# Kernel tuning notes

Measured on AMD Instinct MI355X. Metric: run time of the kernel, lower is better.

Reference implementation:

```python
import jax, jax.numpy as jnp
import numpy as np

# Concrete MACE layer instantiation: hidden irreps = F x (0e + 1o)
N, E, F, R, S, H = 20000, 320000, 64, 8, 10, 64
P = 5                      # CG tensor-product paths for (0e+1o) x (0e+1o)
AVG_NEIGH = 16.0
INV_SQRT3 = 1.0 / np.sqrt(3.0).astype(np.float32)
INV_SQRT2 = 1.0 / np.sqrt(2.0).astype(np.float32)


def setup_inputs() -> dict:
    key = jax.random.key(0)
    ks = jax.random.split(key, 24)
    rn = lambda k, shp, sc=1.0: jax.random.normal(k, shp, dtype=jnp.float32) * sc
    y = jax.random.normal(ks[2], (E, 3), dtype=jnp.float32)
    Y1 = y / jnp.linalg.norm(y, axis=-1, keepdims=True)  # unit spherical harmonics l=1
    return dict(
        s=rn(ks[0], (N, F)),                 # scalar node feats (0e)
        v=rn(ks[1], (N, F, 3)),              # vector node feats (1o)
        Y1=Y1,
        edge_feats=rn(ks[3], (E, R)),        # radial basis
        node_specie=jax.random.randint(ks[4], (N,), 0, S),
        senders=jax.random.randint(ks[5], (E,), 0, N),
        receivers=jax.random.randint(ks[6], (E,), 0, N),
        W_lin_s=rn(ks[7], (F, F), F ** -0.5),
        W_lin_v=rn(ks[8], (F, F), F ** -0.5),
        W_sc_s=rn(ks[9], (S, F, F), F ** -0.5),   # species-dependent skip
        W_sc_v=rn(ks[10], (S, F, F), F ** -0.5),
        W_rad1=rn(ks[11], (R, H), R ** -0.5),     # radial MLP
        W_rad2=rn(ks[12], (H, P * F), H ** -0.5),
        W_int_s=rn(ks[13], (F, F), F ** -0.5),    # post-aggregation linear
        W_int_v=rn(ks[14], (F, F), F ** -0.5),
        w_prod_s=rn(ks[15], (S, 5, F)),           # product-basis species weights (0e out)
        w_prod_v=rn(ks[16], (S, 4, F)),           # product-basis species weights (1o out)
        W_prod_s=rn(ks[17], (F, F), F ** -0.5),
        W_prod_v=rn(ks[18], (F, F), F ** -0.5),
        W_read=rn(ks[19], (F, 1), F ** -0.5),     # linear readout to 0e
    )


def reference(s, v, Y1, edge_feats, node_specie, senders, receivers,
              W_lin_s, W_lin_v, W_sc_s, W_sc_v, W_rad1, W_rad2,
              W_int_s, W_int_v, w_prod_s, w_prod_v, W_prod_s, W_prod_v, W_read):
    n = s.shape[0]
    # --- interaction block: linear up ---
    s1 = s @ W_lin_s                              # [N,F]
    v1 = jnp.einsum('nfc,fg->ngc', v, W_lin_v)    # [N,F,3]
    # species-dependent residual skip connection
    sc_s = jnp.einsum('nf,nfg->ng', s, W_sc_s[node_specie])
    sc_v = jnp.einsum('nfc,nfg->ngc', v, W_sc_v[node_specie])
    # radial MLP -> per-edge, per-path, per-channel tensor-product weights
    h = jax.nn.silu(edge_feats @ W_rad1)
    tw = (h @ W_rad2).reshape(-1, P, F)           # [E,P,F]
    # gather sender features onto edges
    ss = s1[senders]                              # [E,F]
    vs = v1[senders]                              # [E,F,3]
    # CG tensor product with edge spherical harmonics (Y0 == const)
    dot = jnp.einsum('efc,ec->ef', vs, Y1)        # 1o x 1o -> 0e
    crs = jnp.cross(vs, Y1[:, None, :])           # 1o x 1o -> 1o
    m_s = tw[:, 0] * ss + tw[:, 1] * dot * INV_SQRT3                     # [E,F]
    m_v = (tw[:, 2, :, None] * ss[..., None] * Y1[:, None, :]            # 0e x 1o -> 1o
           + tw[:, 3, :, None] * vs                                      # 1o x 0e -> 1o
           + tw[:, 4, :, None] * crs * INV_SQRT2)                        # [E,F,3]
    # scatter-sum over edges to receiver nodes
    A_s = jax.ops.segment_sum(m_s, receivers, num_segments=n)
    A_v = jax.ops.segment_sum(m_v, receivers, num_segments=n)
    # linear to interaction irreps + neighbor normalization (epsilon is None)
    inv = 1.0 / jnp.sqrt(jnp.asarray(AVG_NEIGH, s.dtype))
    A_s = (A_s @ W_int_s) * inv
    A_v = jnp.einsum('nfc,fg->ngc', A_v, W_int_v) * inv
    # --- equivariant product basis (symmetric contraction, correlation=3) ---
    ws = w_prod_s[node_specie]                    # [N,5,F]
    wv = w_prod_v[node_specie]                    # [N,4,F]
    d = jnp.sum(A_v * A_v, axis=-1)               # v.v invariant [N,F]
    B_s = (ws[:, 0] * A_s + ws[:, 1] * A_s * A_s + ws[:, 2] * d
           + ws[:, 3] * A_s ** 3 + ws[:, 4] * A_s * d)
    B_v = (wv[:, 0] + wv[:, 1] * A_s + wv[:, 2] * A_s * A_s + wv[:, 3] * d)[..., None] * A_v
    s_out = B_s @ W_prod_s + sc_s
    v_out = jnp.einsum('nfc,fg->ngc', B_v, W_prod_v) + sc_v
    # --- linear readout (not last layer): invariant per-node output ---
    node_outputs = s_out @ W_read                 # [N,1]
    return node_outputs, s_out, v_out
```

## Files before the change

### kernel.cpp

```cpp
#include <hip/hip_runtime.h>

#define NNODES 20000
#define NEDGES 320000
#define NTILES 1260

typedef __attribute__((ext_vector_type(8))) short short8;
typedef __attribute__((ext_vector_type(4))) float float4v;
typedef _Float16 half2v __attribute__((ext_vector_type(2)));

#define CW2   0
#define CWls  2560
#define CWlv  3072
#define CWis  3584
#define CWiv  4096
#define CWps  4608
#define CWpv  5120
#define CWss  5632
#define CWsv  10752
#define NCHUNK_TOT 15872

__device__ __forceinline__ float bitsf(unsigned u){ union{unsigned u; float f;} x; x.u=u; return x.f; }
__device__ __forceinline__ float b2f(unsigned short u){ return bitsf(((unsigned)u)<<16); }
__device__ __forceinline__ unsigned short f2b(float f){
    union{float f; unsigned u;} x; x.f=f;
    unsigned r = x.u + 0x7fffu + ((x.u>>16)&1u);
    return (unsigned short)(r>>16);
}
__device__ __forceinline__ short8 pack8(const float* f){
    short8 r;
    #pragma unroll
    for (int j=0;j<8;++j) r[j] = (short)f2b(f[j]);
    return r;
}

__constant__ float kINV_SQRT3 = 0.5773502691896258f;
__constant__ float kINV_SQRT2 = 0.7071067811865476f;
__constant__ float kINV_AVG   = 0.25f;

__global__ __launch_bounds__(256) void kprep(
    const int* __restrict__ specie,
    const float* __restrict__ Wr2,
    const float* __restrict__ Wls, const float* __restrict__ Wlv,
    const float* __restrict__ Wis, const float* __restrict__ Wiv,
    const float* __restrict__ Wps, const float* __restrict__ Wpv,
    const float* __restrict__ Wss, const float* __restrict__ Wsv,
    unsigned short* __restrict__ P,
    int* __restrict__ perm, int* __restrict__ tspec)
{
    const int tid = threadIdx.x;
    if (blockIdx.x == 0){
        __shared__ int cnt[10], base[10], ntl[10], cur[10];
        if (tid < 10) cnt[tid] = 0;
        __syncthreads();
        for (int n = tid; n < NNODES; n += 256) atomicAdd(&cnt[specie[n]], 1);
        __syncthreads();
        if (tid == 0){
            int b = 0;
            for (int sp = 0; sp < 10; ++sp){
                base[sp] = b; cur[sp] = b;
                ntl[sp] = (cnt[sp] + 15) >> 4;
                b += ntl[sp] << 4;
            }
        }
        __syncthreads();
        for (int i = tid; i < NTILES*16; i += 256) perm[i] = -1;
        for (int t = tid; t < NTILES; t += 256){
            int sp = 0;
            #pragma unroll
            for (int k = 0; k < 10; ++k)
                if (t >= (base[k] >> 4) && t < (base[k] >> 4) + ntl[k]) sp = k;
            tspec[t] = sp;
        }
        __syncthreads();
        for (int n = tid; n < NNODES; n += 256){
            int slot = atomicAdd(&cur[specie[n]], 1);
            perm[slot] = n;
        }
        return;
    }
    const int c = (blockIdx.x - 1)*256 + tid;
    if (c >= NCHUNK_TOT) return;
    unsigned short t[8];
    if (c < 2560){
        const int nt = c >> 7, ks = (c >> 6) & 1, ln = c & 63;
        const int col = nt*16 + (ln & 15);
        const int jb  = ks*32 + ((ln >> 4) & 3)*8;
        #pragma unroll
        for (int jj = 0; jj < 8; ++jj) t[jj] = f2b(Wr2[(jb+jj)*320 + col]);
    } else {
        int c2 = c - 2560;
        const float* src;
        if      (c2 <  512){ src = Wls; }
        else if (c2 < 1024){ src = Wlv; c2 -= 512; }
        else if (c2 < 1536){ src = Wis; c2 -= 1024; }
        else if (c2 < 2048){ src = Wiv; c2 -= 1536; }
        else if (c2 < 2560){ src = Wps; c2 -= 2048; }
        else if (c2 < 3072){ src = Wpv; c2 -= 2560; }
        else if (c2 < 8192){ src = Wss; c2 -= 3072; }
        else               { src = Wsv; c2 -= 8192; }
        const int grp = c2 >> 9, loc = c2 & 511;
        const int nt = loc >> 7, ks = (loc >> 6) & 1, ln = loc & 63;
        const int col  = nt*16 + (ln & 15);
        const int row0 = grp*64 + ks*32 + ((ln>>4)&3)*8;
        #pragma unroll
        for (int jj = 0; jj < 8; ++jj) t[jj] = f2b(src[(row0+jj)*64 + col]);
    }
    unsigned* d = (unsigned*)(P + (size_t)c*8);
    d[0] = (unsigned)t[0] | ((unsigned)t[1]<<16);
    d[1] = (unsigned)t[2] | ((unsigned)t[3]<<16);
    d[2] = (unsigned)t[4] | ((unsigned)t[5]<<16);
    d[3] = (unsigned)t[6] | ((unsigned)t[7]<<16);
}

__global__ __launch_bounds__(256) void knodeA2(
    const float* __restrict__ s, const float* __restrict__ v,
    const unsigned short* __restrict__ P,
    unsigned short* __restrict__ s1, unsigned short* __restrict__ v1,
    float4v* __restrict__ AhZ)
{
    float4v zz = {0.f,0.f,0.f,0.f};
    for (int i = blockIdx.x*256 + threadIdx.x; i < NNODES*32; i += 313*256) AhZ[i] = zz;

    const int w = threadIdx.x >> 6, lane = threadIdx.x & 63;
    const int t = blockIdx.x*4 + w;
    if (t >= 1250) return;
    const int mcol = lane & 15, quad = lane >> 4;
    const int node = t*16 + mcol;
    const short8* PB = (const short8*)P;

    short8 fS[2], fV[3][2];
    #pragma unroll
    for (int ks = 0; ks < 2; ++ks){
        const int k0 = ks*32 + quad*8;
        float ts[8];
        { float4v a = *(const float4v*)&s[node*64 + k0];
          float4v b = *(const float4v*)&s[node*64 + k0 + 4];
          #pragma unroll
          for (int j = 0; j < 4; ++j){ ts[j] = a[j]; ts[4+j] = b[j]; } }
        fS[ks] = pack8(ts);
        float tv[24];
        #pragma unroll
        for (int q = 0; q < 6; ++q){
            float4v x = *(const float4v*)&v[(node*64 + k0)*3 + q*4];
            #pragma unroll
            for (int j = 0; j < 4; ++j) tv[q*4+j] = x[j];
        }
        #pragma unroll
        for (int c = 0; c < 3; ++c){
            float tc[8];
            #pragma unroll
            for (int j = 0; j < 8; ++j) tc[j] = tv[j*3 + c];
            fV[c][ks] = pack8(tc);
        }
    }
    float4v z = {0.f,0.f,0.f,0.f};
    #pragma unroll
    for (int nt = 0; nt < 4; ++nt){
        float4v aS = __builtin_amdgcn_mfma_f32_16x16x32_bf16(fS[0], PB[CWls+(nt*2+0)*64+lane], z, 0,0,0);
        aS = __builtin_amdgcn_mfma_f32_16x16x32_bf16(fS[1], PB[CWls+(nt*2+1)*64+lane], aS, 0,0,0);
        float4v aV[3];
        #pragma unroll
        for (int c = 0; c < 3; ++c){
            aV[c] = __builtin_amdgcn_mfma_f32_16x16x32_bf16(fV[c][0], PB[CWlv+(nt*2+0)*64+lane], z, 0,0,0);
            aV[c] = __builtin_amdgcn_mfma_f32_16x16x32_bf16(fV[c][1], PB[CWlv+(nt*2+1)*64+lane], aV[c], 0,0,0);
        }
        const int g = nt*16 + mcol;
        #pragma unroll
        for (int r = 0; r < 4; ++r){
            const int nr = t*16 + quad*4 + r;
            s1[nr*64 + g] = f2b(aS[r]);
            #pragma unroll
            for (int c = 0; c < 3; ++c) v1[(nr*3+c)*64 + g] = f2b(aV[c][r]);
        }
    }
}

__global__ __launch_bounds__(256) void kedge2(
    const float* __restrict__ Y1, const float* __restrict__ ef,
    const int* __restrict__ senders, const int* __restrict__ receivers,
    const float* __restrict__ Wr1, const unsigned short* __restrict__ W2s,
    const unsigned short* __restrict__ s1, const unsigned short* __restrict__ v1,
    half2v* __restrict__ Ah)
{
    __shared__ unsigned short hlds[64*72];
    __shared__ unsigned short twlds[64*330];
    const int lane = threadIdx.x & 63;
    const int w    = threadIdx.x >> 6;
    const int ew   = blockIdx.x*64 + w*16;

    float ef0 = ef[ew*8 + lane];
    float ef1 = ef[ew*8 + 64 + lane];
    float w1r[8];
    #pragma unroll
    for (int r = 0; r < 8; ++r) w1r[r] = Wr1[r*64 + lane];
    float yreg  = (lane < 48) ? Y1[ew*3 + lane] : 0.f;
    int sndreg  = (lane < 16) ? senders[ew + lane]   : 0;
    int rcvreg  = (lane < 16) ? receivers[ew + lane] : 0;
    #pragma unroll
    for (int e16 = 0; e16 < 16; ++e16){
        float src = (e16 < 8) ? ef0 : ef1;
        float hj = 0.f;
        #pragma unroll
        for (int r = 0; r < 8; ++r) hj += __shfl(src, (e16&7)*8 + r) * w1r[r];
        hj = hj / (1.f + __expf(-hj));
        hlds[(w*16 + e16)*72 + lane] = f2b(hj);
    }
    __syncthreads();

    short8 a0 = *(const short8*)&hlds[(w*16 + (lane&15))*72 +      (lane>>4)*8];
    short8 a1 = *(const short8*)&hlds[(w*16 + (lane&15))*72 + 32 + (lane>>4)*8];
    float4v acc[20];
    #pragma unroll
    for (int nt = 0; nt < 20; ++nt){
        short8 b0 = *(const short8*)&W2s[((nt*2+0)*64 + lane)*8];
        short8 b1 = *(const short8*)&W2s[((nt*2+1)*64 + lane)*8];
        float4v z = {0.f, 0.f, 0.f, 0.f};
        acc[nt] = __builtin_amdgcn_mfma_f32_16x16x32_bf16(a0, b0, z, 0, 0, 0);
        acc[nt] = __builtin_amdgcn_mfma_f32_16x16x32_bf16(a1, b1, acc[nt], 0, 0, 0);
    }
    #pragma unroll
    for (int nt = 0; nt < 20; ++nt){
        const int col = nt*16 + (lane & 15);
        #pragma unroll
        for (int r = 0; r < 4; ++r){
            const int erow = w*16 + (lane>>4)*4 + r;
            twlds[erow*330 + col] = f2b(acc[nt][r]);
        }
    }

    for (int e16 = 0; e16 < 16; ++e16){
        const int erow = w*16 + e16;
        float tw0 = b2f(twlds[erow*330 +   0 + lane]);
        float tw1 = b2f(twlds[erow*330 +  64 + lane]);
        float tw2 = b2f(twlds[erow*330 + 128 + lane]);
        float tw3 = b2f(twlds[erow*330 + 192 + lane]);
        float tw4 = b2f(twlds[erow*330 + 256 + lane]);
        const int snd = __shfl(sndreg, e16);
        const int rcv = __shfl(rcvreg, e16);
        float y0 = __shfl(yreg, e16*3+0);
        float y1 = __shfl(yreg, e16*3+1);
        float y2 = __shfl(yreg, e16*3+2);
        float ss  = b2f(s1[snd*64 + lane]);
        float vs0 = b2f(v1[(snd*3+0)*64 + lane]);
        float vs1 = b2f(v1[(snd*3+1)*64 + lane]);
        float vs2 = b2f(v1[(snd*3+2)*64 + lane]);
        float dot = vs0*y0 + vs1*y1 + vs2*y2;
        float c0 = vs1*y2 - vs2*y1;
        float c1 = vs2*y0 - vs0*y2;
        float c2 = vs0*y1 - vs1*y0;
        float ms  = tw0*ss + tw1*dot*kINV_SQRT3;
        float t2s = tw2*ss, t4 = tw4*kINV_SQRT2;
        float mv0 = t2s*y0 + tw3*vs0 + t4*c0;
        float mv1 = t2s*y1 + tw3*vs1 + t4*c1;
        float mv2 = t2s*y2 + tw3*vs2 + t4*c2;
        half2v p01 = { (_Float16)ms,  (_Float16)mv0 };
        half2v p23 = { (_Float16)mv1, (_Float16)mv2 };
        __builtin_amdgcn_global_atomic_fadd_v2f16(&Ah[rcv*128 + lane],      p01);
        __builtin_amdgcn_global_atomic_fadd_v2f16(&Ah[rcv*128 + 64 + lane], p23);
    }
}

__global__ __launch_bounds__(256) void knodeC2(
    const float* __restrict__ s, const float* __restrict__ v,
    const half2v* __restrict__ Ah,
    const unsigned short* __restrict__ P,
    const int* __restrict__ perm, const int* __restrict__ tspec,
    const float* __restrict__ wps, const float* __restrict__ wpv,
    const float* __restrict__ Wread,
    float* __restrict__ out)
{
    __shared__ unsigned short Bt[4][4][16*72];
    const int w = threadIdx.x >> 6, lane = threadIdx.x & 63;
    const int t = blockIdx.x*4 + w;
    if (t >= NTILES) return;
    const int mcol = lane & 15, quad = lane >> 4;
    const int spec = tspec[t];
    const int nA   = perm[t*16 + mcol];
    const short8* PB = (const short8*)P;
    const int sb = CWss + spec*512, vb = CWsv + spec*512;

    short8 fAs[2], fAv[3][2], fS[2], fV[3][2];
    if (nA >= 0){
        #pragma unroll
        for (int ks = 0; ks < 2; ++ks){
            const int k0 = ks*32 + quad*8;
            half2v pa[8], pb[8];
            *(float4v*)&pa[0] = *(const float4v*)&Ah[nA*128 + k0];
            *(float4v*)&pa[4] = *(const float4v*)&Ah[nA*128 + k0 + 4];
            *(float4v*)&pb[0] = *(const float4v*)&Ah[nA*128 + 64 + k0];
            *(float4v*)&pb[4] = *(const float4v*)&Ah[nA*128 + 64 + k0 + 4];
            float as_[8], a0_[8], a1_[8], a2_[8];
            #pragma unroll
            for (int j = 0; j < 8; ++j){
                as_[j] = (float)pa[j].x; a0_[j] = (float)pa[j].y;
                a1_[j] = (float)pb[j].x; a2_[j] = (float)pb[j].y;
            }
            fAs[ks] = pack8(as_); fAv[0][ks] = pack8(a0_);
            fAv[1][ks] = pack8(a1_); fAv[2][ks] = pack8(a2_);
            float ts[8];
            { float4v a = *(const float4v*)&s[nA*64 + k0];
              float4v b = *(const float4v*)&s[nA*64 + k0 + 4];
              #pragma unroll
              for (int j = 0; j < 4; ++j){ ts[j] = a[j]; ts[4+j] = b[j]; } }
            fS[ks] = pack8(ts);
            float tv[24];
            #pragma unroll
            for (int q = 0; q < 6; ++q){
                float4v x = *(const float4v*)&v[(nA*64 + k0)*3 + q*4];
                #pragma unroll
                for (int j = 0; j < 4; ++j) tv[q*4+j] = x[j];
            }
            #pragma unroll
            for (int c = 0; c < 3; ++c){
                float tc[8];
                #pragma unroll
                for (int j = 0; j < 8; ++j) tc[j] = tv[j*3 + c];
                fV[c][ks] = pack8(tc);
            }
        }
    } else {
        short8 z8 = {};
        #pragma unroll
        for (int ks = 0; ks < 2; ++ks){
            fAs[ks] = z8; fS[ks] = z8;
            #pragma unroll
            for (int c = 0; c < 3; ++c){ fAv[c][ks] = z8; fV[c][ks] = z8; }
        }
    }

    float4v z = {0.f,0.f,0.f,0.f};
    float4v scS[4], scV[3][4];
    #pragma unroll
    for (int nt = 0; nt < 4; ++nt){
        float4v Ais = __builtin_amdgcn_mfma_f32_16x16x32_bf16(fAs[0], PB[CWis+(nt*2+0)*64+lane], z, 0,0,0);
        Ais = __builtin_amdgcn_mfma_f32_16x16x32_bf16(fAs[1], PB[CWis+(nt*2+1)*64+lane], Ais, 0,0,0);
        float4v Aiv[3];
        #pragma unroll
        for (int c = 0; c < 3; ++c){
            Aiv[c] = __builtin_amdgcn_mfma_f32_16x16x32_bf16(fAv[c][0], PB[CWiv+(nt*2+0)*64+lane], z, 0,0,0);
            Aiv[c] = __builtin_amdgcn_mfma_f32_16x16x32_bf16(fAv[c][1], PB[CWiv+(nt*2+1)*64+lane], Aiv[c], 0,0,0);
        }
        scS[nt] = __builtin_amdgcn_mfma_f32_16x16x32_bf16(fS[0], PB[sb+(nt*2+0)*64+lane], z, 0,0,0);
        scS[nt] = __builtin_amdgcn_mfma_f32_16x16x32_bf16(fS[1], PB[sb+(nt*2+1)*64+lane], scS[nt], 0,0,0);
        #pragma unroll
        for (int c = 0; c < 3; ++c){
            scV[c][nt] = __builtin_amdgcn_mfma_f32_16x16x32_bf16(fV[c][0], PB[vb+(nt*2+0)*64+lane], z, 0,0,0);
            scV[c][nt] = __builtin_amdgcn_mfma_f32_16x16x32_bf16(fV[c][1], PB[vb+(nt*2+1)*64+lane], scV[c][nt], 0,0,0);
        }
        const int g = nt*16 + mcol;
        float w0 = wps[spec*320 +   0 + g], w1 = wps[spec*320 +  64 + g];
        float w2 = wps[spec*320 + 128 + g], w3 = wps[spec*320 + 192 + g];
        float w4 = wps[spec*320 + 256 + g];
        float u0 = wpv[spec*256 +   0 + g], u1 = wpv[spec*256 +  64 + g];
        float u2 = wpv[spec*256 + 128 + g], u3 = wpv[spec*256 + 192 + g];
        #pragma unroll
        for (int r = 0; r < 4; ++r){
            float A  = Ais[r]    * kINV_AVG;
            float a0 = Aiv[0][r] * kINV_AVG;
            float a1 = Aiv[1][r] * kINV_AVG;
            float a2 = Aiv[2][r] * kINV_AVG;
            float d   = a0*a0 + a1*a1 + a2*a2;
            float as2 = A*A;
            float Bs  = w0*A + w1*as2 + w2*d + w3*as2*A + w4*A*d;
            float gg  = u0 + u1*A + u2*as2 + u3*d;
            const int row = quad*4 + r;
            Bt[w][0][row*72 + g] = f2b(Bs);
            Bt[w][1][row*72 + g] = f2b(gg*a0);
            Bt[w][2][row*72 + g] = f2b(gg*a1);
            Bt[w][3][row*72 + g] = f2b(gg*a2);
        }
    }

    short8 bS[2], bV[3][2];
    #pragma unroll
    for (int ks = 0; ks < 2; ++ks){
        bS[ks] = *(const short8*)&Bt[w][0][mcol*72 + ks*32 + quad*8];
        #pragma unroll
        for (int c = 0; c < 3; ++c)
            bV[c][ks] = *(const short8*)&Bt[w][1+c][mcol*72 + ks*32 + quad*8];
    }

    float* out_node = out;
    float* out_s    = out + NNODES;
    float* out_v    = out + NNODES + NNODES*64;
    int ndr[4];
    #pragma unroll
    for (int r = 0; r < 4; ++r) ndr[r] = perm[t*16 + quad*4 + r];
    float4v rd = {0.f,0.f,0.f,0.f};
    #pragma unroll
    for (int nt = 0; nt < 4; ++nt){
        float4v oS = scS[nt];
        oS = __builtin_amdgcn_mfma_f32_16x16x32_bf16(bS[0], PB[CWps+(nt*2+0)*64+lane], oS, 0,0,0);
        oS = __builtin_amdgcn_mfma_f32_16x16x32_bf16(bS[1], PB[CWps+(nt*2+1)*64+lane], oS, 0,0,0);
        float4v oV[3];
        #pragma unroll
        for (int c = 0; c < 3; ++c){
            oV[c] = scV[c][nt];
            oV[c] = __builtin_amdgcn_mfma_f32_16x16x32_bf16(bV[c][0], PB[CWpv+(nt*2+0)*64+lane], oV[c], 0,0,0);
            oV[c] = __builtin_amdgcn_mfma_f32_16x16x32_bf16(bV[c][1], PB[CWpv+(nt*2+1)*64+lane], oV[c], 0,0,0);
        }
        const int g = nt*16 + mcol;
        float wr = Wread[g];
        #pragma unroll
        for (int r = 0; r < 4; ++r){
            if (ndr[r] >= 0){
                out_s[ndr[r]*64 + g] = oS[r];
                #pragma unroll
                for (int c = 0; c < 3; ++c) out_v[(ndr[r]*64 + g)*3 + c] = oV[c][r];
            }
            rd[r] += oS[r] * wr;
        }
    }
    #pragma unroll
    for (int off = 1; off < 16; off <<= 1){
        #pragma unroll
        for (int r = 0; r < 4; ++r) rd[r] += __shfl_xor(rd[r], off);
    }
    if (mcol == 0){
        #pragma unroll
        for (int r = 0; r < 4; ++r) if (ndr[r] >= 0) out_node[ndr[r]] = rd[r];
    }
}

extern "C" void kernel_launch(void* const* d_in, const int* in_sizes, int n_in,
                              void* d_out, int out_size, void* d_ws, size_t ws_size,
                              hipStream_t stream)
{
    (void)in_sizes; (void)n_in; (void)out_size; (void)ws_size;
    const float* s    = (const float*)d_in[0];
    const float* v    = (const float*)d_in[1];
    const float* Y1   = (const float*)d_in[2];
    const float* ef   = (const float*)d_in[3];
    const int* specie = (const int*)d_in[4];
    const int* senders   = (const int*)d_in[5];
    const int* receivers = (const int*)d_in[6];
    const float* Wls  = (const float*)d_in[7];
    const float* Wlv  = (const float*)d_in[8];
    const float* Wss  = (const float*)d_in[9];
    const float* Wsv  = (const float*)d_in[10];
    const float* Wr1  = (const float*)d_in[11];
    const float* Wr2  = (const float*)d_in[12];
    const float* Wis  = (const float*)d_in[13];
    const float* Wiv  = (const float*)d_in[14];
    const float* wps  = (const float*)d_in[15];
    const float* wpv  = (const float*)d_in[16];
    const float* Wps  = (const float*)d_in[17];
    const float* Wpv  = (const float*)d_in[18];
    const float* Wrd  = (const float*)d_in[19];

    float* out = (float*)d_out;
    unsigned short* t_s1 = (unsigned short*)(out + NNODES);
    unsigned short* t_v1 = t_s1 + NNODES*64;

    char* ws = (char*)d_ws;
    unsigned short* P = (unsigned short*)ws;
    half2v* Ah  = (half2v*)(ws + 262144);
    int* perm   = (int*)(ws + 10502144);
    int* tspec  = (int*)(ws + 10582784);

    kprep<<<63, 256, 0, stream>>>(specie, Wr2, Wls, Wlv, Wis, Wiv, Wps, Wpv, Wss, Wsv,
                                  P, perm, tspec);
    knodeA2<<<313, 256, 0, stream>>>(s, v, P, t_s1, t_v1, (float4v*)Ah);
    kedge2<<<5000, 256, 0, stream>>>(Y1, ef, senders, receivers, Wr1, P + CW2*8, t_s1, t_v1, Ah);
    knodeC2<<<315, 256, 0, stream>>>(s, v, Ah, P, perm, tspec, wps, wpv, Wrd, out);
}
```

Measured before the change: 331.1 us.

## Sort edges by receiver and coalesce per-receiver atomics in edge kernel

Builds a counting-sort permutation of edges by receiver (count in knodeA2, serial single-block scan, scatter kernel) and has the edge kernel process edges in that order. Consecutive edges with the same receiver accumulate messages in registers and issue one pair of packed fp16 atomics per run instead of per edge. This targets atomic traffic and contention on the aggregation buffer. In exchange it adds two launches, a single-block scan, gathered (non-coalesced) reads of edge features, Y1 and sender indices through the permutation, and a nondeterministic edge order within each receiver. With about 16 edges per receiver, each 16-edge wave covers only one or two receivers.

Result: slower. 374.0 us (+12.9%).

```diff
diff --git a/kernel.cpp b/kernel.cpp
--- a/kernel.cpp
+++ b/kernel.cpp
@@ -45,9 +45,12 @@
     const float* __restrict__ Wps, const float* __restrict__ Wpv,
     const float* __restrict__ Wss, const float* __restrict__ Wsv,
     unsigned short* __restrict__ P,
-    int* __restrict__ perm, int* __restrict__ tspec)
+    int* __restrict__ perm, int* __restrict__ tspec,
+    int* __restrict__ ecnt)
 {
     const int tid = threadIdx.x;
+    for (int i = blockIdx.x*256 + tid; i < NNODES; i += 63*256) ecnt[i] = 0;
+
     if (blockIdx.x == 0){
         __shared__ int cnt[10], base[10], ntl[10], cur[10];
         if (tid < 10) cnt[tid] = 0;
@@ -115,11 +118,14 @@
 __global__ __launch_bounds__(256) void knodeA2(
     const float* __restrict__ s, const float* __restrict__ v,
     const unsigned short* __restrict__ P,
+    const int* __restrict__ receivers, int* __restrict__ ecnt,
     unsigned short* __restrict__ s1, unsigned short* __restrict__ v1,
     float4v* __restrict__ AhZ)
 {
     float4v zz = {0.f,0.f,0.f,0.f};
     for (int i = blockIdx.x*256 + threadIdx.x; i < NNODES*32; i += 313*256) AhZ[i] = zz;
+    for (int e = blockIdx.x*256 + threadIdx.x; e < NEDGES; e += 313*256)
+        atomicAdd(&ecnt[receivers[e]], 1);
 
     const int w = threadIdx.x >> 6, lane = threadIdx.x & 63;
     const int t = blockIdx.x*4 + w;
@@ -175,11 +181,48 @@
     }
 }
 
+__global__ __launch_bounds__(256) void kscan(int* __restrict__ ecnt)
+{
+    __shared__ int part[256];
+    const int tid  = threadIdx.x;
+    const int base = tid*79;
+    int sum = 0;
+    #pragma unroll 1
+    for (int i = 0; i < 79; ++i){
+        int idx = base + i;
+        if (idx < NNODES) sum += ecnt[idx];
+    }
+    part[tid] = sum;
+    __syncthreads();
+    if (tid == 0){
+        int acc = 0;
+        #pragma unroll 1
+        for (int i = 0; i < 256; ++i){ int c = part[i]; part[i] = acc; acc += c; }
+    }
+    __syncthreads();
+    int run = part[tid];
+    #pragma unroll 1
+    for (int i = 0; i < 79; ++i){
+        int idx = base + i;
+        if (idx < NNODES){ int c = ecnt[idx]; ecnt[idx] = run; run += c; }
+    }
+}
+
+__global__ __launch_bounds__(256) void kscat(
+    const int* __restrict__ receivers, int* __restrict__ ecur, int* __restrict__ eperm)
+{
+    const int e = blockIdx.x*256 + threadIdx.x;
+    if (e >= NEDGES) return;
+    const int pos = atomicAdd(&ecur[receivers[e]], 1);
+    eperm[pos] = e;
+}
+
 __global__ __launch_bounds__(256) void kedge2(
     const float* __restrict__ Y1, const float* __restrict__ ef,
     const int* __restrict__ senders, const int* __restrict__ receivers,
     const float* __restrict__ Wr1, const unsigned short* __restrict__ W2s,
     const unsigned short* __restrict__ s1, const unsigned short* __restrict__ v1,
+    const int* __restrict__ eperm,
     half2v* __restrict__ Ah)
 {
     __shared__ unsigned short hlds[64*72];
@@ -188,20 +231,32 @@
     const int w    = threadIdx.x >> 6;
     const int ew   = blockIdx.x*64 + w*16;
 
-    float ef0 = ef[ew*8 + lane];
-    float ef1 = ef[ew*8 + 64 + lane];
+    int epreg = 0;
+    if (lane < 16) epreg = eperm[ew + lane];
+    const int  eme = __shfl(epreg, lane >> 2);
+    const float efa = ef[eme*8 + (lane&3)*2];
+    const float efb = ef[eme*8 + (lane&3)*2 + 1];
+
     float w1r[8];
     #pragma unroll
     for (int r = 0; r < 8; ++r) w1r[r] = Wr1[r*64 + lane];
-    float yreg  = (lane < 48) ? Y1[ew*3 + lane] : 0.f;
-    int sndreg  = (lane < 16) ? senders[ew + lane]   : 0;
-    int rcvreg  = (lane < 16) ? receivers[ew + lane] : 0;
+
+    float y0r = 0.f, y1r = 0.f, y2r = 0.f;
+    int   sndreg = 0, rcvreg = 0;
+    if (lane < 16){
+        y0r = Y1[epreg*3 + 0];
+        y1r = Y1[epreg*3 + 1];
+        y2r = Y1[epreg*3 + 2];
+        sndreg = senders[epreg];
+        rcvreg = receivers[epreg];
+    }
+
     #pragma unroll
     for (int e16 = 0; e16 < 16; ++e16){
-        float src = (e16 < 8) ? ef0 : ef1;
         float hj = 0.f;
         #pragma unroll
-        for (int r = 0; r < 8; ++r) hj += __shfl(src, (e16&7)*8 + r) * w1r[r];
+        for (int r = 0; r < 8; ++r)
+            hj += __shfl((r&1) ? efb : efa, e16*4 + (r>>1)) * w1r[r];
         hj = hj / (1.f + __expf(-hj));
         hlds[(w*16 + e16)*72 + lane] = f2b(hj);
     }
@@ -228,6 +283,8 @@
         }
     }
 
+    int   cur = -1;
+    float aS = 0.f, aV0 = 0.f, aV1 = 0.f, aV2 = 0.f;
     for (int e16 = 0; e16 < 16; ++e16){
         const int erow = w*16 + e16;
         float tw0 = b2f(twlds[erow*330 +   0 + lane]);
@@ -237,9 +294,9 @@
         float tw4 = b2f(twlds[erow*330 + 256 + lane]);
         const int snd = __shfl(sndreg, e16);
         const int rcv = __shfl(rcvreg, e16);
-        float y0 = __shfl(yreg, e16*3+0);
-        float y1 = __shfl(yreg, e16*3+1);
-        float y2 = __shfl(yreg, e16*3+2);
+        float y0 = __shfl(y0r, e16);
+        float y1 = __shfl(y1r, e16);
+        float y2 = __shfl(y2r, e16);
         float ss  = b2f(s1[snd*64 + lane]);
         float vs0 = b2f(v1[(snd*3+0)*64 + lane]);
         float vs1 = b2f(v1[(snd*3+1)*64 + lane]);
@@ -253,10 +310,23 @@
         float mv0 = t2s*y0 + tw3*vs0 + t4*c0;
         float mv1 = t2s*y1 + tw3*vs1 + t4*c1;
         float mv2 = t2s*y2 + tw3*vs2 + t4*c2;
-        half2v p01 = { (_Float16)ms,  (_Float16)mv0 };
-        half2v p23 = { (_Float16)mv1, (_Float16)mv2 };
-        __builtin_amdgcn_global_atomic_fadd_v2f16(&Ah[rcv*128 + lane],      p01);
-        __builtin_amdgcn_global_atomic_fadd_v2f16(&Ah[rcv*128 + 64 + lane], p23);
+        if (rcv != cur){
+            if (cur >= 0){
+                half2v p01 = { (_Float16)aS,  (_Float16)aV0 };
+                half2v p23 = { (_Float16)aV1, (_Float16)aV2 };
+                __builtin_amdgcn_global_atomic_fadd_v2f16(&Ah[cur*128 + lane],      p01);
+                __builtin_amdgcn_global_atomic_fadd_v2f16(&Ah[cur*128 + 64 + lane], p23);
+            }
+            cur = rcv;
+            aS = 0.f; aV0 = 0.f; aV1 = 0.f; aV2 = 0.f;
+        }
+        aS += ms; aV0 += mv0; aV1 += mv1; aV2 += mv2;
+    }
+    if (cur >= 0){
+        half2v p01 = { (_Float16)aS,  (_Float16)aV0 };
+        half2v p23 = { (_Float16)aV1, (_Float16)aV2 };
+        __builtin_amdgcn_global_atomic_fadd_v2f16(&Ah[cur*128 + lane],      p01);
+        __builtin_amdgcn_global_atomic_fadd_v2f16(&Ah[cur*128 + 64 + lane], p23);
     }
 }
 
@@ -451,6 +521,8 @@
     float* out = (float*)d_out;
     unsigned short* t_s1 = (unsigned short*)(out + NNODES);
     unsigned short* t_v1 = t_s1 + NNODES*64;
+    int* ecnt  = (int*)(out + 2600000);
+    int* eperm = (int*)(out + 2624000);
 
     char* ws = (char*)d_ws;
     unsigned short* P = (unsigned short*)ws;
@@ -459,8 +531,10 @@
     int* tspec  = (int*)(ws + 10582784);
 
     kprep<<<63, 256, 0, stream>>>(specie, Wr2, Wls, Wlv, Wis, Wiv, Wps, Wpv, Wss, Wsv,
-                                  P, perm, tspec);
-    knodeA2<<<313, 256, 0, stream>>>(s, v, P, t_s1, t_v1, (float4v*)Ah);
-    kedge2<<<5000, 256, 0, stream>>>(Y1, ef, senders, receivers, Wr1, P + CW2*8, t_s1, t_v1, Ah);
+                                  P, perm, tspec, ecnt);
+    knodeA2<<<313, 256, 0, stream>>>(s, v, P, receivers, ecnt, t_s1, t_v1, (float4v*)Ah);
+    kscan<<<1, 256, 0, stream>>>(ecnt);
+    kscat<<<1250, 256, 0, stream>>>(receivers, ecnt, eperm);
+    kedge2<<<5000, 256, 0, stream>>>(Y1, ef, senders, receivers, Wr1, P + CW2*8, t_s1, t_v1, eperm, Ah);
     knodeC2<<<315, 256, 0, stream>>>(s, v, Ah, P, perm, tspec, wps, wpv, Wrd, out);
 }
```

## Interleave sender s/v features and prefetch them before edge MLP

Applied to the files above, without the earlier changes.

Stores each node's scalar and three vector bf16 features interleaved, so the edge kernel fetches one 8-byte vector per lane instead of four scattered 2-byte loads. The 16 sender gathers are issued at kernel start, before the radial MLP and MFMA work, so their latency overlaps that compute. A minimum-occupancy hint of three blocks is added to kedge2. The prefetch array adds registers, and the occupancy bound may force spills.

Result: no change. 329.7 us (-0.4%).

```diff
diff --git a/kernel.cpp b/kernel.cpp
--- a/kernel.cpp
+++ b/kernel.cpp
@@ -6,6 +6,7 @@
 
 typedef __attribute__((ext_vector_type(8))) short short8;
 typedef __attribute__((ext_vector_type(4))) float float4v;
+typedef __attribute__((ext_vector_type(4))) unsigned short ushort4v;
 typedef _Float16 half2v __attribute__((ext_vector_type(2)));
 
 #define CW2   0
@@ -115,7 +116,7 @@
 __global__ __launch_bounds__(256) void knodeA2(
     const float* __restrict__ s, const float* __restrict__ v,
     const unsigned short* __restrict__ P,
-    unsigned short* __restrict__ s1, unsigned short* __restrict__ v1,
+    unsigned short* __restrict__ sv1,
     float4v* __restrict__ AhZ)
 {
     float4v zz = {0.f,0.f,0.f,0.f};
@@ -168,18 +169,17 @@
         #pragma unroll
         for (int r = 0; r < 4; ++r){
             const int nr = t*16 + quad*4 + r;
-            s1[nr*64 + g] = f2b(aS[r]);
-            #pragma unroll
-            for (int c = 0; c < 3; ++c) v1[(nr*3+c)*64 + g] = f2b(aV[c][r]);
-        }
-    }
-}
-
-__global__ __launch_bounds__(256) void kedge2(
+            ushort4v pk = { f2b(aS[r]), f2b(aV[0][r]), f2b(aV[1][r]), f2b(aV[2][r]) };
+            *(ushort4v*)&sv1[(size_t)(nr*64 + g)*4] = pk;
+        }
+    }
+}
+
+__global__ __launch_bounds__(256, 3) void kedge2(
     const float* __restrict__ Y1, const float* __restrict__ ef,
     const int* __restrict__ senders, const int* __restrict__ receivers,
     const float* __restrict__ Wr1, const unsigned short* __restrict__ W2s,
-    const unsigned short* __restrict__ s1, const unsigned short* __restrict__ v1,
+    const unsigned short* __restrict__ sv1,
     half2v* __restrict__ Ah)
 {
     __shared__ unsigned short hlds[64*72];
@@ -196,6 +196,14 @@
     float yreg  = (lane < 48) ? Y1[ew*3 + lane] : 0.f;
     int sndreg  = (lane < 16) ? senders[ew + lane]   : 0;
     int rcvreg  = (lane < 16) ? receivers[ew + lane] : 0;
+
+    ushort4v svp[16];
+    #pragma unroll
+    for (int e16 = 0; e16 < 16; ++e16){
+        const int snd = __shfl(sndreg, e16);
+        svp[e16] = *(const ushort4v*)&sv1[(size_t)(snd*64 + lane)*4];
+    }
+
     #pragma unroll
     for (int e16 = 0; e16 < 16; ++e16){
         float src = (e16 < 8) ? ef0 : ef1;
@@ -235,15 +243,15 @@
         float tw2 = b2f(twlds[erow*330 + 128 + lane]);
         float tw3 = b2f(twlds[erow*330 + 192 + lane]);
         float tw4 = b2f(twlds[erow*330 + 256 + lane]);
-        const int snd = __shfl(sndreg, e16);
         const int rcv = __shfl(rcvreg, e16);
         float y0 = __shfl(yreg, e16*3+0);
         float y1 = __shfl(yreg, e16*3+1);
         float y2 = __shfl(yreg, e16*3+2);
-        float ss  = b2f(s1[snd*64 + lane]);
-        float vs0 = b2f(v1[(snd*3+0)*64 + lane]);
-        float vs1 = b2f(v1[(snd*3+1)*64 + lane]);
-        float vs2 = b2f(v1[(snd*3+2)*64 + lane]);
+        const ushort4v q = svp[e16];
+        float ss  = b2f(q[0]);
+        float vs0 = b2f(q[1]);
+        float vs1 = b2f(q[2]);
+        float vs2 = b2f(q[3]);
         float dot = vs0*y0 + vs1*y1 + vs2*y2;
         float c0 = vs1*y2 - vs2*y1;
         float c1 = vs2*y0 - vs0*y2;
@@ -449,8 +457,7 @@
     const float* Wrd  = (const float*)d_in[19];
 
     float* out = (float*)d_out;
-    unsigned short* t_s1 = (unsigned short*)(out + NNODES);
-    unsigned short* t_v1 = t_s1 + NNODES*64;
+    unsigned short* t_sv = (unsigned short*)(out + NNODES);
 
     char* ws = (char*)d_ws;
     unsigned short* P = (unsigned short*)ws;
@@ -460,7 +467,7 @@
 
     kprep<<<63, 256, 0, stream>>>(specie, Wr2, Wls, Wlv, Wis, Wiv, Wps, Wpv, Wss, Wsv,
                                   P, perm, tspec);
-    knodeA2<<<313, 256, 0, stream>>>(s, v, P, t_s1, t_v1, (float4v*)Ah);
-    kedge2<<<5000, 256, 0, stream>>>(Y1, ef, senders, receivers, Wr1, P + CW2*8, t_s1, t_v1, Ah);
+    knodeA2<<<313, 256, 0, stream>>>(s, v, P, t_sv, (float4v*)Ah);
+    kedge2<<<5000, 256, 0, stream>>>(Y1, ef, senders, receivers, Wr1, P + CW2*8, t_sv, Ah);
     knodeC2<<<315, 256, 0, stream>>>(s, v, Ah, P, perm, tspec, wps, wpv, Wrd, out);
 }
```
